# Performance work log

Measured on AMD Instinct MI355X. Metric: run time of the kernel, lower is better.

Reference implementation:

```python
import jax, jax.numpy as jnp
import numpy as np

N, E, D = 100000, 1600000, 128
EPS = 1e-5


def _bn(h, g, b):
    m = h.mean(0)
    v = ((h - m) ** 2).mean(0)  # biased var, as torch BatchNorm1d normalization
    return g * (h - m) / jnp.sqrt(v + EPS) + b


def _sage(x, src, dst, w_self, w_neigh, b, n):
    # mean aggregation over in-neighbors (edges src->dst)
    agg = jax.ops.segment_sum(x[src], dst, num_segments=n)          # [N, D]
    cnt = jax.ops.segment_sum(jnp.ones(src.shape, x.dtype), dst, num_segments=n)
    mean = agg / jnp.maximum(cnt, 1.0)[:, None]
    return x @ w_self + mean @ w_neigh + b


def setup_inputs() -> dict:
    key = jax.random.key(0)
    ks = jax.random.split(key, 8)
    s = 1.0 / np.sqrt(D)
    return {
        "x": jax.random.normal(ks[0], (N, D), jnp.float32),
        "src": jax.random.randint(ks[1], (E,), 0, N, jnp.int32),
        "dst": jax.random.randint(ks[2], (E,), 0, N, jnp.int32),
        "w_self1": jax.random.normal(ks[3], (D, D), jnp.float32) * s,
        "w_neigh1": jax.random.normal(ks[4], (D, D), jnp.float32) * s,
        "b1": jnp.zeros((D,), jnp.float32),
        "w_self2": jax.random.normal(ks[5], (D, D), jnp.float32) * s,
        "w_neigh2": jax.random.normal(ks[6], (D, D), jnp.float32) * s,
        "b2": jnp.zeros((D,), jnp.float32),
        "w_skip": jax.random.normal(ks[7], (D, D), jnp.float32) * s,
        "b_skip": jnp.zeros((D,), jnp.float32),
        "g1": jnp.ones((D,), jnp.float32), "be1": jnp.zeros((D,), jnp.float32),
        "g2": jnp.ones((D,), jnp.float32), "be2": jnp.zeros((D,), jnp.float32),
        "g3": jnp.ones((D,), jnp.float32), "be3": jnp.zeros((D,), jnp.float32),
    }


def reference(x, src, dst, w_self1, w_neigh1, b1, w_self2, w_neigh2, b2,
              w_skip, b_skip, g1, be1, g2, be2, g3, be3):
    n = x.shape[0]
    h1 = _sage(x, src, dst, w_self1, w_neigh1, b1, n)
    h1 = jax.nn.relu(_bn(h1, g1, be1))           # dropout: eval-mode identity
    h2 = _sage(h1, src, dst, w_self2, w_neigh2, b2, n)
    h2 = _bn(h2, g2, be2)
    skip = _bn(h1 @ w_skip + b_skip, g3, be3)
    return jax.nn.relu(h2 + skip)
```

## Files before the change

kernel.cpp:

```cpp
#include <hip/hip_runtime.h>

#define D 128
#define PCHUNK 4096
#define SCAP 8192

typedef short bf16x8 __attribute__((ext_vector_type(8)));
typedef float f32x4 __attribute__((ext_vector_type(4)));

__device__ __forceinline__ ushort f2b(float f){
  unsigned u = __builtin_bit_cast(unsigned, f);
  u += 0x7fffu + ((u >> 16) & 1u);
  return (ushort)(u >> 16);
}
__device__ __forceinline__ float b2f(ushort h){
  unsigned u = ((unsigned)h) << 16;
  return __builtin_bit_cast(float, u);
}

__global__ __launch_bounds__(256) void k_p0(const int* __restrict__ dst,
                                            int* __restrict__ bcnt, int E){
  __shared__ int h[512];
  for (int u=threadIdx.x; u<512; u+=256) h[u]=0;
  __syncthreads();
  for (long long i=(long long)blockIdx.x*256+threadIdx.x; i<E; i+=(long long)gridDim.x*256)
    atomicAdd(&h[dst[i]>>8], 1);
  __syncthreads();
  for (int u=threadIdx.x; u<512; u+=256) if (h[u]) atomicAdd(&bcnt[u], h[u]);
}

__global__ void k_bscan(const int* __restrict__ bcnt, int* __restrict__ bbase,
                        int* __restrict__ bcur, int nb, int E){
  __shared__ int sh[1024];
  int t = threadIdx.x;
  int v = (t<nb) ? bcnt[t] : 0;
  sh[t]=v; __syncthreads();
  for (int off=1; off<1024; off<<=1){
    int add = (t>=off)?sh[t-off]:0;
    __syncthreads();
    sh[t]+=add;
    __syncthreads();
  }
  if (t<nb){ int e=sh[t]-v; bbase[t]=e; bcur[t]=e; }
  if (t==nb) bbase[t]=E;
}

__global__ __launch_bounds__(256) void k_part(const int* __restrict__ src,
        const int* __restrict__ dst, int* __restrict__ bcur,
        unsigned* __restrict__ pairs, int E){
  __shared__ int hist[512], offA[512], offB[512], gbase[512];
  __shared__ int sS[PCHUNK], sD[PCHUNK];
  const int t = threadIdx.x;
  const int base = blockIdx.x * PCHUNK;
  const int cnt = min(PCHUNK, E - base);
  for (int u=t; u<512; u+=256) hist[u]=0;
  __syncthreads();
  int rs[16], rd[16];
  #pragma unroll
  for (int j=0;j<16;j++){
    int li = j*256 + t;
    if (li < cnt){
      rs[j]=src[base+li]; rd[j]=dst[base+li];
      atomicAdd(&hist[rd[j]>>8],1);
    } else { rs[j]=0; rd[j]=-1; }
  }
  __syncthreads();
  int *cur=offA, *nxt=offB;
  for (int u=t; u<512; u+=256) cur[u]=hist[u];
  __syncthreads();
  for (int off=1; off<512; off<<=1){
    for (int u=t; u<512; u+=256) nxt[u] = cur[u] + ((u>=off)?cur[u-off]:0);
    __syncthreads();
    int* tmp=cur; cur=nxt; nxt=tmp;
  }
  for (int u=t; u<512; u+=256) nxt[u] = cur[u]-hist[u];
  __syncthreads();
  #pragma unroll
  for (int j=0;j<16;j++){
    if (j*256+t < cnt){
      int b = rd[j]>>8;
      int p = atomicAdd(&nxt[b],1);
      sS[p]=rs[j]; sD[p]=rd[j];
    }
  }
  __syncthreads();
  for (int u=t; u<512; u+=256){
    int c = hist[u];
    if (c>0) gbase[u] = atomicAdd(&bcur[u], c);
  }
  __syncthreads();
  #pragma unroll
  for (int j=0;j<16;j++){
    int idx = j*256+t;
    if (idx<cnt){
      int d = sD[idx]; int b = d>>8;
      int gpos = gbase[b] + (idx - (cur[b]-hist[b]));
      pairs[gpos] = (unsigned)sS[idx] | ((unsigned)(d & 255) << 24);
    }
  }
}

__global__ __launch_bounds__(256) void k_sortb(const unsigned* __restrict__ pairs,
        const int* __restrict__ bbase, int* __restrict__ offs,
        int* __restrict__ slots, int N, int NB){
  __shared__ int nh[256], nc[256], sc[256];
  __shared__ int stage[SCAP];
  const int b = blockIdx.x, t = threadIdx.x;
  const int base = bbase[b];
  const int cnt  = bbase[b+1] - base;
  nh[t]=0; __syncthreads();
  for (int i=t;i<cnt;i+=256) atomicAdd(&nh[pairs[base+i] >> 24],1);
  __syncthreads();
  int v = nh[t];
  sc[t]=v; __syncthreads();
  for (int off=1; off<256; off<<=1){
    int add = (t>=off)?sc[t-off]:0;
    __syncthreads();
    sc[t]+=add;
    __syncthreads();
  }
  int excl = sc[t]-v;
  nc[t]=excl;
  int node = (b<<8)+t;
  if (node<N) offs[node]=base+excl;
  if (b==NB-1 && t==0) offs[N]=bbase[NB];
  __syncthreads();
  if (cnt<=SCAP){
    for (int i=t;i<cnt;i+=256){
      unsigned p = pairs[base+i];
      int pos = atomicAdd(&nc[p >> 24],1);
      stage[pos]=(int)(p & 0xffffffu);
    }
    __syncthreads();
    for (int i=t;i<cnt;i+=256) slots[base+i]=stage[i];
  } else {
    for (int i=t;i<cnt;i+=256){
      unsigned p = pairs[base+i];
      int pos = atomicAdd(&nc[p >> 24],1);
      slots[base+pos]=(int)(p & 0xffffffu);
    }
  }
}

__global__ __launch_bounds__(256) void k_xcast(const float* __restrict__ x,
                                               ushort* __restrict__ xb, long long n4){
  long long i = (long long)blockIdx.x*256 + threadIdx.x;
  const long long stride = (long long)gridDim.x*256;
  for (; i < n4; i += stride){
    float4 v = reinterpret_cast<const float4*>(x)[i];
    ushort4 o;
    o.x = f2b(v.x); o.y = f2b(v.y); o.z = f2b(v.z); o.w = f2b(v.w);
    reinterpret_cast<ushort4*>(xb)[i] = o;
  }
}

__global__ __launch_bounds__(256) void k_wtall(
    const float* __restrict__ w_self1, const float* __restrict__ w_neigh1,
    const float* __restrict__ w_self2, const float* __restrict__ w_neigh2,
    const float* __restrict__ w_skip,
    ushort* __restrict__ Wb1, ushort* __restrict__ Wb2, ushort* __restrict__ Wb3){
  const int grp = blockIdx.x >> 6;
  const int idx = (blockIdx.x & 63)*256 + threadIdx.x;
  const int k = idx >> 7, c = idx & 127;
  const float* W; ushort* Wb; int K, k0;
  switch (grp){
    case 0: W=w_self1;  Wb=Wb1; K=256; k0=0;   break;
    case 1: W=w_neigh1; Wb=Wb1; K=256; k0=128; break;
    case 2: W=w_self2;  Wb=Wb2; K=256; k0=0;   break;
    case 3: W=w_neigh2; Wb=Wb2; K=256; k0=128; break;
    default:W=w_skip;   Wb=Wb3; K=128; k0=0;   break;
  }
  Wb[(size_t)c*K + k0 + k] = f2b(W[idx]);
}

__global__ __launch_bounds__(256) void k_gatherb(const ushort* __restrict__ Xb,
        const int* __restrict__ slots, const int* __restrict__ offs,
        ushort* __restrict__ meanb, int N){
  int node = blockIdx.x*4 + (threadIdx.x >> 6);
  int c2 = (threadIdx.x & 63) * 2;
  if (node >= N) return;
  const int beg = offs[node], end = offs[node+1];
  float sx0=0,sy0=0,sx1=0,sy1=0,sx2=0,sy2=0,sx3=0,sy3=0;
  int j = beg;
  while (j < end && (j & 3)){
    unsigned u = *reinterpret_cast<const unsigned*>(&Xb[(size_t)slots[j]*D + c2]);
    sx0 += b2f((ushort)u); sy0 += b2f((ushort)(u>>16));
    ++j;
  }
  const int nfull = (end - j) >> 2;
  const int4* sp = reinterpret_cast<const int4*>(slots + j);

#define G8(ia, ib) { \
    unsigned u0 = *reinterpret_cast<const unsigned*>(&Xb[(size_t)(ia).x*D + c2]); \
    unsigned u1 = *reinterpret_cast<const unsigned*>(&Xb[(size_t)(ia).y*D + c2]); \
    unsigned u2 = *reinterpret_cast<const unsigned*>(&Xb[(size_t)(ia).z*D + c2]); \
    unsigned u3 = *reinterpret_cast<const unsigned*>(&Xb[(size_t)(ia).w*D + c2]); \
    unsigned u4 = *reinterpret_cast<const unsigned*>(&Xb[(size_t)(ib).x*D + c2]); \
    unsigned u5 = *reinterpret_cast<const unsigned*>(&Xb[(size_t)(ib).y*D + c2]); \
    unsigned u6 = *reinterpret_cast<const unsigned*>(&Xb[(size_t)(ib).z*D + c2]); \
    unsigned u7 = *reinterpret_cast<const unsigned*>(&Xb[(size_t)(ib).w*D + c2]); \
    sx0 += b2f((ushort)u0); sy0 += b2f((ushort)(u0>>16)); \
    sx1 += b2f((ushort)u1); sy1 += b2f((ushort)(u1>>16)); \
    sx2 += b2f((ushort)u2); sy2 += b2f((ushort)(u2>>16)); \
    sx3 += b2f((ushort)u3); sy3 += b2f((ushort)(u3>>16)); \
    sx0 += b2f((ushort)u4); sy0 += b2f((ushort)(u4>>16)); \
    sx1 += b2f((ushort)u5); sy1 += b2f((ushort)(u5>>16)); \
    sx2 += b2f((ushort)u6); sy2 += b2f((ushort)(u6>>16)); \
    sx3 += b2f((ushort)u7); sy3 += b2f((ushort)(u7>>16)); }

  int g = 0;
  if (nfull >= 2){
    int4 ia = sp[0], ib = sp[1];
    for (g = 2; g + 2 <= nfull; g += 2){
      int4 na = sp[g], nb = sp[g+1];
      G8(ia, ib);
      ia = na; ib = nb;
    }
    G8(ia, ib);
  }
  if (g < nfull){
    int4 ia = sp[g];
    unsigned u0 = *reinterpret_cast<const unsigned*>(&Xb[(size_t)ia.x*D + c2]);
    unsigned u1 = *reinterpret_cast<const unsigned*>(&Xb[(size_t)ia.y*D + c2]);
    unsigned u2 = *reinterpret_cast<const unsigned*>(&Xb[(size_t)ia.z*D + c2]);
    unsigned u3 = *reinterpret_cast<const unsigned*>(&Xb[(size_t)ia.w*D + c2]);
    sx0 += b2f((ushort)u0); sy0 += b2f((ushort)(u0>>16));
    sx1 += b2f((ushort)u1); sy1 += b2f((ushort)(u1>>16));
    sx2 += b2f((ushort)u2); sy2 += b2f((ushort)(u2>>16));
    sx3 += b2f((ushort)u3); sy3 += b2f((ushort)(u3>>16));
  }
  j += 4*nfull;
  for (; j < end; ++j){
    unsigned u = *reinterpret_cast<const unsigned*>(&Xb[(size_t)slots[j]*D + c2]);
    sx0 += b2f((ushort)u); sy0 += b2f((ushort)(u>>16));
  }
#undef G8
  float deg = (float)(end - beg);
  float rc = deg > 0.f ? 1.0f/deg : 0.f;
  unsigned o = (unsigned)f2b((sx0+sx1+sx2+sx3)*rc)
             | ((unsigned)f2b((sy0+sy1+sy2+sy3)*rc) << 16);
  *reinterpret_cast<unsigned*>(&meanb[(size_t)node*D + c2]) = o;
}

template<bool SKIP>
__global__ __launch_bounds__(256, 1) void k_mfma(
    const ushort* __restrict__ A0, const ushort* __restrict__ A1,
    const ushort* __restrict__ Wb, const ushort* __restrict__ Wk,
    const float* __restrict__ bias, const float* __restrict__ biasK,
    ushort* __restrict__ C, ushort* __restrict__ Ck,
    float* __restrict__ gS, float* __restrict__ gQ,
    float* __restrict__ gSK, float* __restrict__ gQK, int N, int NT)
{
  __shared__ ushort Wt8[8][128][40];
  __shared__ ushort Wkt4[SKIP ? 4*128*40 : 1];
  __shared__ ushort At[2][128][40];
  __shared__ float shS[128], shQ[128], shSK[SKIP?128:1], shQK[SKIP?128:1];
  const int tid = threadIdx.x;
  if (tid < 128){ shS[tid]=0.f; shQ[tid]=0.f; if (SKIP){ shSK[tid]=0.f; shQK[tid]=0.f; } }
  const int bid = blockIdx.x, gridN = gridDim.x;
  const int lane = tid & 63, wid = tid >> 6;
  const int wr = wid >> 1, wc = wid & 1;
  const int lr = lane & 15, kq = lane >> 4;
  const int sr4 = tid >> 2, s8 = (tid & 3) * 8;

  #pragma unroll
  for (int s=0;s<8;s++){
    *reinterpret_cast<int4*>(&Wt8[s][sr4][s8]) =
        *reinterpret_cast<const int4*>(&Wb[(size_t)sr4*256 + s*32 + s8]);
    *reinterpret_cast<int4*>(&Wt8[s][sr4+64][s8]) =
        *reinterpret_cast<const int4*>(&Wb[(size_t)(sr4+64)*256 + s*32 + s8]);
  }
  if (SKIP){
    #pragma unroll
    for (int s=0;s<4;s++){
      *reinterpret_cast<int4*>(&Wkt4[((s*128) + sr4)*40 + s8]) =
          *reinterpret_cast<const int4*>(&Wk[(size_t)sr4*128 + s*32 + s8]);
      *reinterpret_cast<int4*>(&Wkt4[((s*128) + sr4 + 64)*40 + s8]) =
          *reinterpret_cast<const int4*>(&Wk[(size_t)(sr4+64)*128 + s*32 + s8]);
    }
  }

  int4 va0a,va0b, va1a,va1b, va2a,va2b, va3a,va3b;

#define LOADA(S, GT, TT) { \
    int gr0_ = (GT)*128 + sr4;      if (gr0_ >= N) gr0_ = N-1; \
    int gr1_ = (GT)*128 + sr4 + 64; if (gr1_ >= N) gr1_ = N-1; \
    const ushort* As_ = ((TT) >= 4) ? A1 : A0; \
    const int ka_ = ((TT) & 3) * 32; \
    va##S##a = *reinterpret_cast<const int4*>(&As_[(size_t)gr0_*D + ka_ + s8]); \
    va##S##b = *reinterpret_cast<const int4*>(&As_[(size_t)gr1_*D + ka_ + s8]); }

#define WRITEA(S, BW) { \
    *reinterpret_cast<int4*>(&At[BW][sr4][s8]) = va##S##a; \
    *reinterpret_cast<int4*>(&At[BW][sr4+64][s8]) = va##S##b; }

#define PBAR() { asm volatile("s_waitcnt lgkmcnt(0)" ::: "memory"); \
    __builtin_amdgcn_s_barrier(); __builtin_amdgcn_sched_barrier(0); }

#define STEPBODY(BR, TT, WITHK, ...) { \
    bf16x8 af0 = *reinterpret_cast<const bf16x8*>(&At[BR][64*wr + lr][kq*8]); \
    bf16x8 af1 = *reinterpret_cast<const bf16x8*>(&At[BR][64*wr + 16 + lr][kq*8]); \
    bf16x8 af2 = *reinterpret_cast<const bf16x8*>(&At[BR][64*wr + 32 + lr][kq*8]); \
    bf16x8 af3 = *reinterpret_cast<const bf16x8*>(&At[BR][64*wr + 48 + lr][kq*8]); \
    bf16x8 bw0 = *reinterpret_cast<const bf16x8*>(&Wt8[TT][64*wc + lr][kq*8]); \
    bf16x8 bw1 = *reinterpret_cast<const bf16x8*>(&Wt8[TT][64*wc + 16 + lr][kq*8]); \
    bf16x8 bw2 = *reinterpret_cast<const bf16x8*>(&Wt8[TT][64*wc + 32 + lr][kq*8]); \
    bf16x8 bw3 = *reinterpret_cast<const bf16x8*>(&Wt8[TT][64*wc + 48 + lr][kq*8]); \
    bf16x8 bk0{}, bk1{}, bk2{}, bk3{}; \
    if (SKIP && (WITHK)){ \
      bk0 = *reinterpret_cast<const bf16x8*>(&Wkt4[(((TT)&3)*128 + 64*wc + lr)*40 + kq*8]); \
      bk1 = *reinterpret_cast<const bf16x8*>(&Wkt4[(((TT)&3)*128 + 64*wc + 16 + lr)*40 + kq*8]); \
      bk2 = *reinterpret_cast<const bf16x8*>(&Wkt4[(((TT)&3)*128 + 64*wc + 32 + lr)*40 + kq*8]); \
      bk3 = *reinterpret_cast<const bf16x8*>(&Wkt4[(((TT)&3)*128 + 64*wc + 48 + lr)*40 + kq*8]); \
    } \
    __VA_ARGS__; \
    __builtin_amdgcn_s_setprio(1); \
    acc[0][0] = __builtin_amdgcn_mfma_f32_16x16x32_bf16(af0, bw0, acc[0][0], 0,0,0); \
    acc[0][1] = __builtin_amdgcn_mfma_f32_16x16x32_bf16(af0, bw1, acc[0][1], 0,0,0); \
    acc[0][2] = __builtin_amdgcn_mfma_f32_16x16x32_bf16(af0, bw2, acc[0][2], 0,0,0); \
    acc[0][3] = __builtin_amdgcn_mfma_f32_16x16x32_bf16(af0, bw3, acc[0][3], 0,0,0); \
    acc[1][0] = __builtin_amdgcn_mfma_f32_16x16x32_bf16(af1, bw0, acc[1][0], 0,0,0); \
    acc[1][1] = __builtin_amdgcn_mfma_f32_16x16x32_bf16(af1, bw1, acc[1][1], 0,0,0); \
    acc[1][2] = __builtin_amdgcn_mfma_f32_16x16x32_bf16(af1, bw2, acc[1][2], 0,0,0); \
    acc[1][3] = __builtin_amdgcn_mfma_f32_16x16x32_bf16(af1, bw3, acc[1][3], 0,0,0); \
    acc[2][0] = __builtin_amdgcn_mfma_f32_16x16x32_bf16(af2, bw0, acc[2][0], 0,0,0); \
    acc[2][1] = __builtin_amdgcn_mfma_f32_16x16x32_bf16(af2, bw1, acc[2][1], 0,0,0); \
    acc[2][2] = __builtin_amdgcn_mfma_f32_16x16x32_bf16(af2, bw2, acc[2][2], 0,0,0); \
    acc[2][3] = __builtin_amdgcn_mfma_f32_16x16x32_bf16(af2, bw3, acc[2][3], 0,0,0); \
    acc[3][0] = __builtin_amdgcn_mfma_f32_16x16x32_bf16(af3, bw0, acc[3][0], 0,0,0); \
    acc[3][1] = __builtin_amdgcn_mfma_f32_16x16x32_bf16(af3, bw1, acc[3][1], 0,0,0); \
    acc[3][2] = __builtin_amdgcn_mfma_f32_16x16x32_bf16(af3, bw2, acc[3][2], 0,0,0); \
    acc[3][3] = __builtin_amdgcn_mfma_f32_16x16x32_bf16(af3, bw3, acc[3][3], 0,0,0); \
    if (SKIP && (WITHK)){ \
      accK[0][0] = __builtin_amdgcn_mfma_f32_16x16x32_bf16(af0, bk0, accK[0][0], 0,0,0); \
      accK[0][1] = __builtin_amdgcn_mfma_f32_16x16x32_bf16(af0, bk1, accK[0][1], 0,0,0); \
      accK[0][2] = __builtin_amdgcn_mfma_f32_16x16x32_bf16(af0, bk2, accK[0][2], 0,0,0); \
      accK[0][3] = __builtin_amdgcn_mfma_f32_16x16x32_bf16(af0, bk3, accK[0][3], 0,0,0); \
      accK[1][0] = __builtin_amdgcn_mfma_f32_16x16x32_bf16(af1, bk0, accK[1][0], 0,0,0); \
      accK[1][1] = __builtin_amdgcn_mfma_f32_16x16x32_bf16(af1, bk1, accK[1][1], 0,0,0); \
      accK[1][2] = __builtin_amdgcn_mfma_f32_16x16x32_bf16(af1, bk2, accK[1][2], 0,0,0); \
      accK[1][3] = __builtin_amdgcn_mfma_f32_16x16x32_bf16(af1, bk3, accK[1][3], 0,0,0); \
      accK[2][0] = __builtin_amdgcn_mfma_f32_16x16x32_bf16(af2, bk0, accK[2][0], 0,0,0); \
      accK[2][1] = __builtin_amdgcn_mfma_f32_16x16x32_bf16(af2, bk1, accK[2][1], 0,0,0); \
      accK[2][2] = __builtin_amdgcn_mfma_f32_16x16x32_bf16(af2, bk2, accK[2][2], 0,0,0); \
      accK[2][3] = __builtin_amdgcn_mfma_f32_16x16x32_bf16(af2, bk3, accK[2][3], 0,0,0); \
      accK[3][0] = __builtin_amdgcn_mfma_f32_16x16x32_bf16(af3, bk0, accK[3][0], 0,0,0); \
      accK[3][1] = __builtin_amdgcn_mfma_f32_16x16x32_bf16(af3, bk1, accK[3][1], 0,0,0); \
      accK[3][2] = __builtin_amdgcn_mfma_f32_16x16x32_bf16(af3, bk2, accK[3][2], 0,0,0); \
      accK[3][3] = __builtin_amdgcn_mfma_f32_16x16x32_bf16(af3, bk3, accK[3][3], 0,0,0); \
    } \
    __builtin_amdgcn_s_setprio(0); }

  f32x4 acc[4][4], accK[SKIP?4:1][SKIP?4:1];
  #pragma unroll
  for (int m=0;m<4;m++)
    #pragma unroll
    for (int n=0;n<4;n++){
      acc[m][n] = (f32x4){0.f,0.f,0.f,0.f};
      if (SKIP) accK[m][n] = (f32x4){0.f,0.f,0.f,0.f};
    }
  float bs[4]={0,0,0,0}, bq[4]={0,0,0,0}, bsk[4]={0,0,0,0}, bqk[4]={0,0,0,0};
  float bv[4], bkv[4];
  #pragma unroll
  for (int n=0;n<4;n++){
    bv[n] = bias[64*wc + 16*n + lr];
    bkv[n] = SKIP ? biasK[64*wc + 16*n + lr] : 0.f;
  }

  {
    const int t0 = bid;
    LOADA(0, t0, 0);
    LOADA(1, t0, 1);
    LOADA(2, t0, 2);
    LOADA(3, t0, 3);
    WRITEA(0, 0);
    PBAR();
  }

  for (int tile = bid; tile < NT; tile += gridN){
    const int tnext = tile + gridN;
    const bool hasnext = (tnext < NT);
    STEPBODY(0, 0, 1, LOADA(0, tile, 4));
    WRITEA(1, 1); PBAR();
    STEPBODY(1, 1, 1, LOADA(1, tile, 5));
    WRITEA(2, 0); PBAR();
    STEPBODY(0, 2, 1, LOADA(2, tile, 6));
    WRITEA(3, 1); PBAR();
    STEPBODY(1, 3, 1, LOADA(3, tile, 7));
    WRITEA(0, 0); PBAR();
    STEPBODY(0, 4, 0, if (hasnext) LOADA(0, tnext, 0));
    WRITEA(1, 1); PBAR();
    STEPBODY(1, 5, 0, if (hasnext) LOADA(1, tnext, 1));
    WRITEA(2, 0); PBAR();
    STEPBODY(0, 6, 0, if (hasnext) LOADA(2, tnext, 2));
    WRITEA(3, 1); PBAR();
    STEPBODY(1, 7, 0, if (hasnext) LOADA(3, tnext, 3));
    if (hasnext){ WRITEA(0, 0); PBAR(); }

    #pragma unroll
    for (int m=0;m<4;m++){
      #pragma unroll
      for (int r=0;r<4;r++){
        int row = tile*128 + 64*wr + 16*m + kq*4 + r;
        if (row < N){
          #pragma unroll
          for (int n=0;n<4;n++){
            int col = 64*wc + 16*n + lr;
            float v = acc[m][n][r] + bv[n];
            C[(size_t)row*D + col] = f2b(v);
            bs[n] += v; bq[n] += v*v;
            if (SKIP){
              float u = accK[m][n][r] + bkv[n];
              Ck[(size_t)row*D + col] = f2b(u);
              bsk[n] += u; bqk[n] += u*u;
            }
          }
        }
      }
    }
    #pragma unroll
    for (int m=0;m<4;m++)
      #pragma unroll
      for (int n=0;n<4;n++){
        acc[m][n] = (f32x4){0.f,0.f,0.f,0.f};
        if (SKIP) accK[m][n] = (f32x4){0.f,0.f,0.f,0.f};
      }
  }
#undef LOADA
#undef WRITEA
#undef PBAR
#undef STEPBODY

  #pragma unroll
  for (int n=0;n<4;n++){
    float s = bs[n], q = bq[n];
    s += __shfl_xor(s,16); s += __shfl_xor(s,32);
    q += __shfl_xor(q,16); q += __shfl_xor(q,32);
    if (kq == 0){
      int col = 64*wc + 16*n + lr;
      atomicAdd(&shS[col], s);
      atomicAdd(&shQ[col], q);
    }
    if (SKIP){
      float sk = bsk[n], qk = bqk[n];
      sk += __shfl_xor(sk,16); sk += __shfl_xor(sk,32);
      qk += __shfl_xor(qk,16); qk += __shfl_xor(qk,32);
      if (kq == 0){
        int col = 64*wc + 16*n + lr;
        atomicAdd(&shSK[col], sk);
        atomicAdd(&shQK[col], qk);
      }
    }
  }
  __syncthreads();
  if (tid < 128){
    unsafeAtomicAdd(&gS[tid], shS[tid]);
    unsafeAtomicAdd(&gQ[tid], shQ[tid]);
    if (SKIP){
      unsafeAtomicAdd(&gSK[tid], shSK[tid]);
      unsafeAtomicAdd(&gQK[tid], shQK[tid]);
    }
  }
}

__global__ __launch_bounds__(256) void k_bnrelub(const ushort* __restrict__ hpre,
      ushort* __restrict__ hb,
      const float* __restrict__ sum, const float* __restrict__ sq,
      const float* __restrict__ g, const float* __restrict__ be,
      float invN, long long n4){
  __shared__ float A[128], B[128];
  if (threadIdx.x < 128){
    int c = threadIdx.x;
    float m = sum[c]*invN;
    float v = sq[c]*invN - m*m;
    float a = g[c]*rsqrtf(fmaxf(v, 0.f) + 1e-5f);
    A[c] = a;
    B[c] = be[c] - m*a;
  }
  __syncthreads();
  long long i = (long long)blockIdx.x*256 + threadIdx.x;
  const long long stride = (long long)gridDim.x*256;
  for (; i < n4; i += stride){
    int c = ((int)(i & 31)) << 2;
    float4 a = *reinterpret_cast<const float4*>(A + c);
    float4 b = *reinterpret_cast<const float4*>(B + c);
    ushort4 hv = reinterpret_cast<const ushort4*>(hpre)[i];
    ushort4 o;
    o.x = f2b(fmaxf(a.x*b2f(hv.x) + b.x, 0.f));
    o.y = f2b(fmaxf(a.y*b2f(hv.y) + b.y, 0.f));
    o.z = f2b(fmaxf(a.z*b2f(hv.z) + b.z, 0.f));
    o.w = f2b(fmaxf(a.w*b2f(hv.w) + b.w, 0.f));
    reinterpret_cast<ushort4*>(hb)[i] = o;
  }
}

__global__ __launch_bounds__(256) void k_final(const ushort* __restrict__ h2,
      const ushort* __restrict__ sk, float* __restrict__ out,
      const float* __restrict__ sum2, const float* __restrict__ sq2,
      const float* __restrict__ g2, const float* __restrict__ be2,
      const float* __restrict__ sum3, const float* __restrict__ sq3,
      const float* __restrict__ g3, const float* __restrict__ be3,
      float invN, long long n4){
  __shared__ float A2[128], B2[128], A3[128], B3[128];
  if (threadIdx.x < 128){
    int c = threadIdx.x;
    float m2 = sum2[c]*invN;
    float v2 = sq2[c]*invN - m2*m2;
    float a2 = g2[c]*rsqrtf(fmaxf(v2, 0.f) + 1e-5f);
    A2[c] = a2; B2[c] = be2[c] - m2*a2;
    float m3 = sum3[c]*invN;
    float v3 = sq3[c]*invN - m3*m3;
    float a3 = g3[c]*rsqrtf(fmaxf(v3, 0.f) + 1e-5f);
    A3[c] = a3; B3[c] = be3[c] - m3*a3;
  }
  __syncthreads();
  long long i = (long long)blockIdx.x*256 + threadIdx.x;
  const long long stride = (long long)gridDim.x*256;
  for (; i < n4; i += stride){
    int c = ((int)(i & 31)) << 2;
    float4 a2 = *reinterpret_cast<const float4*>(A2 + c);
    float4 b2 = *reinterpret_cast<const float4*>(B2 + c);
    float4 a3 = *reinterpret_cast<const float4*>(A3 + c);
    float4 b3 = *reinterpret_cast<const float4*>(B3 + c);
    ushort4 h = reinterpret_cast<const ushort4*>(h2)[i];
    ushort4 s = reinterpret_cast<const ushort4*>(sk)[i];
    float4 v;
    v.x = fmaxf(a2.x*b2f(h.x) + b2.x + a3.x*b2f(s.x) + b3.x, 0.f);
    v.y = fmaxf(a2.y*b2f(h.y) + b2.y + a3.y*b2f(s.y) + b3.y, 0.f);
    v.z = fmaxf(a2.z*b2f(h.z) + b2.z + a3.z*b2f(s.z) + b3.z, 0.f);
    v.w = fmaxf(a2.w*b2f(h.w) + b2.w + a3.w*b2f(s.w) + b3.w, 0.f);
    reinterpret_cast<float4*>(out)[i] = v;
  }
}

extern "C" void kernel_launch(void* const* d_in, const int* in_sizes, int n_in,
                              void* d_out, int out_size, void* d_ws, size_t ws_size,
                              hipStream_t stream) {
  const float* x        = (const float*)d_in[0];
  const int*   src      = (const int*)  d_in[1];
  const int*   dst      = (const int*)  d_in[2];
  const float* w_self1  = (const float*)d_in[3];
  const float* w_neigh1 = (const float*)d_in[4];
  const float* b1       = (const float*)d_in[5];
  const float* w_self2  = (const float*)d_in[6];
  const float* w_neigh2 = (const float*)d_in[7];
  const float* b2       = (const float*)d_in[8];
  const float* w_skip   = (const float*)d_in[9];
  const float* b_skip   = (const float*)d_in[10];
  const float* g1       = (const float*)d_in[11];
  const float* be1      = (const float*)d_in[12];
  const float* g2       = (const float*)d_in[13];
  const float* be2      = (const float*)d_in[14];
  const float* g3       = (const float*)d_in[15];
  const float* be3      = (const float*)d_in[16];
  (void)n_in; (void)ws_size;

  const int N = in_sizes[0] / D;
  const int E = in_sizes[1];
  const int NB = (N + 255) >> 8;
  float* out = (float*)d_out;

  char* p = (char*)d_ws;
  const size_t nd2 = (((size_t)N * D * 2) + 255) / 256 * 256;
  ushort* meanb  = (ushort*)p; p += nd2;
  ushort* h1b    = (ushort*)p; p += nd2;
  ushort* hpre_b = (ushort*)p; p += nd2;
  ushort* skip_b = (ushort*)p; p += nd2;
  ushort* Wb1    = (ushort*)p; p += 256*128*2;
  ushort* Wb2    = (ushort*)p; p += 256*128*2;
  ushort* Wb3    = (ushort*)p; p += 128*128*2;
  int*    offs   = (int*)p;   p += (((size_t)(N+1)*4) + 255) / 256 * 256;
  int*    bcnt   = (int*)p;   p += 2304;
  float*  st     = (float*)p; p += 1536*sizeof(float);
  int*    bbase  = (int*)p;   p += 2304;
  int*    bcur   = (int*)p;   p += 2048;
  float *sum1=st,      *sq1=st+128,  *sum2=st+256, *sq2=st+384, *sum3=st+512, *sq3=st+640;

  const size_t slpad = (((size_t)E*4) + 255) / 256 * 256;
  const size_t xbpad = (((size_t)N*D*2) + 255) / 256 * 256;
  int*      slots = (int*)d_out;
  ushort*   xb    = (ushort*)((char*)d_out + slpad);
  unsigned* pairs = (unsigned*)((char*)d_out + slpad + xbpad);

  hipMemsetAsync(bcnt, 0, 2304 + 1536*sizeof(float), stream);

  const long long n4 = (long long)N * D / 4;

  k_xcast<<<2048, 256, 0, stream>>>(x, xb, n4);
  k_wtall<<<320, 256, 0, stream>>>(w_self1, w_neigh1, w_self2, w_neigh2, w_skip,
                                   Wb1, Wb2, Wb3);

  k_p0<<<1024, 256, 0, stream>>>(dst, bcnt, E);
  k_bscan<<<1, 1024, 0, stream>>>(bcnt, bbase, bcur, NB, E);
  k_part<<<(E + PCHUNK - 1)/PCHUNK, 256, 0, stream>>>(src, dst, bcur, pairs, E);
  k_sortb<<<NB, 256, 0, stream>>>(pairs, bbase, offs, slots, N, NB);

  const int gablocks = (N + 3) / 4;
  const int NT = (N + 127) / 128;
  const int gpersist = 256;
  const float invN = 1.0f / (float)N;

  k_gatherb<<<gablocks, 256, 0, stream>>>(xb, slots, offs, meanb, N);
  k_mfma<false><<<gpersist, 256, 0, stream>>>(xb, meanb, Wb1, nullptr, b1, nullptr,
                                              hpre_b, nullptr, sum1, sq1, nullptr, nullptr, N, NT);
  k_bnrelub<<<4096, 256, 0, stream>>>(hpre_b, h1b, sum1, sq1, g1, be1, invN, n4);

  k_gatherb<<<gablocks, 256, 0, stream>>>(h1b, slots, offs, meanb, N);

  k_mfma<true><<<gpersist, 256, 0, stream>>>(h1b, meanb, Wb2, Wb3, b2, b_skip,
                                             hpre_b, skip_b, sum2, sq2, sum3, sq3, N, NT);

  k_final<<<4096, 256, 0, stream>>>(hpre_b, skip_b, out,
                                    sum2, sq2, g2, be2, sum3, sq3, g3, be3, invN, n4);
}
```

Before: 292.1 us.

## Fuse BN+ReLU of layer 1 into gather and MFMA loads, merge prep kernels

```diff
diff --git a/kernel.cpp b/kernel.cpp
--- a/kernel.cpp
+++ b/kernel.cpp
@@ -17,15 +17,64 @@
   return __builtin_bit_cast(float, u);
 }
 
-__global__ __launch_bounds__(256) void k_p0(const int* __restrict__ dst,
-                                            int* __restrict__ bcnt, int E){
+__device__ __forceinline__ int4 bnpack8(int4 v, float4 a0, float4 a1, float4 b0, float4 b1){
+  unsigned w0=(unsigned)v.x, w1=(unsigned)v.y, w2=(unsigned)v.z, w3=(unsigned)v.w;
+  float x0 = fmaxf(fmaf(a0.x, b2f((ushort)w0),        b0.x), 0.f);
+  float x1 = fmaxf(fmaf(a0.y, b2f((ushort)(w0>>16)),  b0.y), 0.f);
+  float x2 = fmaxf(fmaf(a0.z, b2f((ushort)w1),        b0.z), 0.f);
+  float x3 = fmaxf(fmaf(a0.w, b2f((ushort)(w1>>16)),  b0.w), 0.f);
+  float x4 = fmaxf(fmaf(a1.x, b2f((ushort)w2),        b1.x), 0.f);
+  float x5 = fmaxf(fmaf(a1.y, b2f((ushort)(w2>>16)),  b1.y), 0.f);
+  float x6 = fmaxf(fmaf(a1.z, b2f((ushort)w3),        b1.z), 0.f);
+  float x7 = fmaxf(fmaf(a1.w, b2f((ushort)(w3>>16)),  b1.w), 0.f);
+  int4 r;
+  r.x = (int)((unsigned)f2b(x0) | ((unsigned)f2b(x1)<<16));
+  r.y = (int)((unsigned)f2b(x2) | ((unsigned)f2b(x3)<<16));
+  r.z = (int)((unsigned)f2b(x4) | ((unsigned)f2b(x5)<<16));
+  r.w = (int)((unsigned)f2b(x6) | ((unsigned)f2b(x7)<<16));
+  return r;
+}
+
+__global__ __launch_bounds__(256) void k_prep(
+    const float* __restrict__ w_self1, const float* __restrict__ w_neigh1,
+    const float* __restrict__ w_self2, const float* __restrict__ w_neigh2,
+    const float* __restrict__ w_skip,
+    ushort* __restrict__ Wb1, ushort* __restrict__ Wb2, ushort* __restrict__ Wb3,
+    const int* __restrict__ dst, int* __restrict__ bcnt, int E,
+    const float* __restrict__ x, ushort* __restrict__ xb, long long n4){
   __shared__ int h[512];
-  for (int u=threadIdx.x; u<512; u+=256) h[u]=0;
-  __syncthreads();
-  for (long long i=(long long)blockIdx.x*256+threadIdx.x; i<E; i+=(long long)gridDim.x*256)
-    atomicAdd(&h[dst[i]>>8], 1);
-  __syncthreads();
-  for (int u=threadIdx.x; u<512; u+=256) if (h[u]) atomicAdd(&bcnt[u], h[u]);
+  const int bid = blockIdx.x;
+  if (bid < 320){
+    const int grp = bid >> 6;
+    const int idx = (bid & 63)*256 + threadIdx.x;
+    const int k = idx >> 7, c = idx & 127;
+    const float* W; ushort* Wb; int K, k0;
+    switch (grp){
+      case 0: W=w_self1;  Wb=Wb1; K=256; k0=0;   break;
+      case 1: W=w_neigh1; Wb=Wb1; K=256; k0=128; break;
+      case 2: W=w_self2;  Wb=Wb2; K=256; k0=0;   break;
+      case 3: W=w_neigh2; Wb=Wb2; K=256; k0=128; break;
+      default:W=w_skip;   Wb=Wb3; K=128; k0=0;   break;
+    }
+    Wb[(size_t)c*K + k0 + k] = f2b(W[idx]);
+  } else if (bid < 1344){
+    const int pb = bid - 320;
+    for (int u=threadIdx.x; u<512; u+=256) h[u]=0;
+    __syncthreads();
+    for (long long i=(long long)pb*256+threadIdx.x; i<E; i+=(long long)1024*256)
+      atomicAdd(&h[dst[i]>>8], 1);
+    __syncthreads();
+    for (int u=threadIdx.x; u<512; u+=256) if (h[u]) atomicAdd(&bcnt[u], h[u]);
+  } else {
+    long long i = (long long)(bid-1344)*256 + threadIdx.x;
+    const long long stride = 2048LL*256;
+    for (; i < n4; i += stride){
+      float4 v = reinterpret_cast<const float4*>(x)[i];
+      ushort4 o;
+      o.x = f2b(v.x); o.y = f2b(v.y); o.z = f2b(v.z); o.w = f2b(v.w);
+      reinterpret_cast<ushort4*>(xb)[i] = o;
+    }
+  }
 }
 
 __global__ void k_bscan(const int* __restrict__ bcnt, int* __restrict__ bbase,
@@ -141,49 +190,32 @@
   }
 }
 
-__global__ __launch_bounds__(256) void k_xcast(const float* __restrict__ x,
-                                               ushort* __restrict__ xb, long long n4){
-  long long i = (long long)blockIdx.x*256 + threadIdx.x;
-  const long long stride = (long long)gridDim.x*256;
-  for (; i < n4; i += stride){
-    float4 v = reinterpret_cast<const float4*>(x)[i];
-    ushort4 o;
-    o.x = f2b(v.x); o.y = f2b(v.y); o.z = f2b(v.z); o.w = f2b(v.w);
-    reinterpret_cast<ushort4*>(xb)[i] = o;
-  }
-}
-
-__global__ __launch_bounds__(256) void k_wtall(
-    const float* __restrict__ w_self1, const float* __restrict__ w_neigh1,
-    const float* __restrict__ w_self2, const float* __restrict__ w_neigh2,
-    const float* __restrict__ w_skip,
-    ushort* __restrict__ Wb1, ushort* __restrict__ Wb2, ushort* __restrict__ Wb3){
-  const int grp = blockIdx.x >> 6;
-  const int idx = (blockIdx.x & 63)*256 + threadIdx.x;
-  const int k = idx >> 7, c = idx & 127;
-  const float* W; ushort* Wb; int K, k0;
-  switch (grp){
-    case 0: W=w_self1;  Wb=Wb1; K=256; k0=0;   break;
-    case 1: W=w_neigh1; Wb=Wb1; K=256; k0=128; break;
-    case 2: W=w_self2;  Wb=Wb2; K=256; k0=0;   break;
-    case 3: W=w_neigh2; Wb=Wb2; K=256; k0=128; break;
-    default:W=w_skip;   Wb=Wb3; K=128; k0=0;   break;
-  }
-  Wb[(size_t)c*K + k0 + k] = f2b(W[idx]);
-}
-
+template<bool BN>
 __global__ __launch_bounds__(256) void k_gatherb(const ushort* __restrict__ Xb,
         const int* __restrict__ slots, const int* __restrict__ offs,
-        ushort* __restrict__ meanb, int N){
+        ushort* __restrict__ meanb, int N,
+        const float* __restrict__ sum, const float* __restrict__ sq,
+        const float* __restrict__ g, const float* __restrict__ be, float invN){
   int node = blockIdx.x*4 + (threadIdx.x >> 6);
   int c2 = (threadIdx.x & 63) * 2;
   if (node >= N) return;
+  float a0=0.f,a1=0.f,b0c=0.f,b1c=0.f;
+  if (BN){
+    float m0 = sum[c2]*invN,   m1 = sum[c2+1]*invN;
+    float v0 = sq[c2]*invN - m0*m0, v1 = sq[c2+1]*invN - m1*m1;
+    a0 = g[c2]  *rsqrtf(fmaxf(v0,0.f)+1e-5f);
+    a1 = g[c2+1]*rsqrtf(fmaxf(v1,0.f)+1e-5f);
+    b0c = be[c2]   - m0*a0;
+    b1c = be[c2+1] - m1*a1;
+  }
+#define AX0(x) (BN ? fmaxf(fmaf(a0,(x),b0c),0.f) : (x))
+#define AX1(x) (BN ? fmaxf(fmaf(a1,(x),b1c),0.f) : (x))
   const int beg = offs[node], end = offs[node+1];
   float sx0=0,sy0=0,sx1=0,sy1=0,sx2=0,sy2=0,sx3=0,sy3=0;
   int j = beg;
   while (j < end && (j & 3)){
     unsigned u = *reinterpret_cast<const unsigned*>(&Xb[(size_t)slots[j]*D + c2]);
-    sx0 += b2f((ushort)u); sy0 += b2f((ushort)(u>>16));
+    sx0 += AX0(b2f((ushort)u)); sy0 += AX1(b2f((ushort)(u>>16)));
     ++j;
   }
   const int nfull = (end - j) >> 2;
@@ -198,42 +230,44 @@
     unsigned u5 = *reinterpret_cast<const unsigned*>(&Xb[(size_t)(ib).y*D + c2]); \
     unsigned u6 = *reinterpret_cast<const unsigned*>(&Xb[(size_t)(ib).z*D + c2]); \
     unsigned u7 = *reinterpret_cast<const unsigned*>(&Xb[(size_t)(ib).w*D + c2]); \
-    sx0 += b2f((ushort)u0); sy0 += b2f((ushort)(u0>>16)); \
-    sx1 += b2f((ushort)u1); sy1 += b2f((ushort)(u1>>16)); \
-    sx2 += b2f((ushort)u2); sy2 += b2f((ushort)(u2>>16)); \
-    sx3 += b2f((ushort)u3); sy3 += b2f((ushort)(u3>>16)); \
-    sx0 += b2f((ushort)u4); sy0 += b2f((ushort)(u4>>16)); \
-    sx1 += b2f((ushort)u5); sy1 += b2f((ushort)(u5>>16)); \
-    sx2 += b2f((ushort)u6); sy2 += b2f((ushort)(u6>>16)); \
-    sx3 += b2f((ushort)u7); sy3 += b2f((ushort)(u7>>16)); }
-
-  int g = 0;
+    sx0 += AX0(b2f((ushort)u0)); sy0 += AX1(b2f((ushort)(u0>>16))); \
+    sx1 += AX0(b2f((ushort)u1)); sy1 += AX1(b2f((ushort)(u1>>16))); \
+    sx2 += AX0(b2f((ushort)u2)); sy2 += AX1(b2f((ushort)(u2>>16))); \
+    sx3 += AX0(b2f((ushort)u3)); sy3 += AX1(b2f((ushort)(u3>>16))); \
+    sx0 += AX0(b2f((ushort)u4)); sy0 += AX1(b2f((ushort)(u4>>16))); \
+    sx1 += AX0(b2f((ushort)u5)); sy1 += AX1(b2f((ushort)(u5>>16))); \
+    sx2 += AX0(b2f((ushort)u6)); sy2 += AX1(b2f((ushort)(u6>>16))); \
+    sx3 += AX0(b2f((ushort)u7)); sy3 += AX1(b2f((ushort)(u7>>16))); }
+
+  int g8 = 0;
   if (nfull >= 2){
     int4 ia = sp[0], ib = sp[1];
-    for (g = 2; g + 2 <= nfull; g += 2){
-      int4 na = sp[g], nb = sp[g+1];
+    for (g8 = 2; g8 + 2 <= nfull; g8 += 2){
+      int4 na = sp[g8], nb = sp[g8+1];
       G8(ia, ib);
       ia = na; ib = nb;
     }
     G8(ia, ib);
   }
-  if (g < nfull){
-    int4 ia = sp[g];
+  if (g8 < nfull){
+    int4 ia = sp[g8];
     unsigned u0 = *reinterpret_cast<const unsigned*>(&Xb[(size_t)ia.x*D + c2]);
     unsigned u1 = *reinterpret_cast<const unsigned*>(&Xb[(size_t)ia.y*D + c2]);
     unsigned u2 = *reinterpret_cast<const unsigned*>(&Xb[(size_t)ia.z*D + c2]);
     unsigned u3 = *reinterpret_cast<const unsigned*>(&Xb[(size_t)ia.w*D + c2]);
-    sx0 += b2f((ushort)u0); sy0 += b2f((ushort)(u0>>16));
-    sx1 += b2f((ushort)u1); sy1 += b2f((ushort)(u1>>16));
-    sx2 += b2f((ushort)u2); sy2 += b2f((ushort)(u2>>16));
-    sx3 += b2f((ushort)u3); sy3 += b2f((ushort)(u3>>16));
+    sx0 += AX0(b2f((ushort)u0)); sy0 += AX1(b2f((ushort)(u0>>16)));
+    sx1 += AX0(b2f((ushort)u1)); sy1 += AX1(b2f((ushort)(u1>>16)));
+    sx2 += AX0(b2f((ushort)u2)); sy2 += AX1(b2f((ushort)(u2>>16)));
+    sx3 += AX0(b2f((ushort)u3)); sy3 += AX1(b2f((ushort)(u3>>16)));
   }
   j += 4*nfull;
   for (; j < end; ++j){
     unsigned u = *reinterpret_cast<const unsigned*>(&Xb[(size_t)slots[j]*D + c2]);
-    sx0 += b2f((ushort)u); sy0 += b2f((ushort)(u>>16));
+    sx0 += AX0(b2f((ushort)u)); sy0 += AX1(b2f((ushort)(u>>16)));
   }
 #undef G8
+#undef AX0
+#undef AX1
   float deg = (float)(end - beg);
   float rc = deg > 0.f ? 1.0f/deg : 0.f;
   unsigned o = (unsigned)f2b((sx0+sx1+sx2+sx3)*rc)
@@ -248,12 +282,15 @@
     const float* __restrict__ bias, const float* __restrict__ biasK,
     ushort* __restrict__ C, ushort* __restrict__ Ck,
     float* __restrict__ gS, float* __restrict__ gQ,
-    float* __restrict__ gSK, float* __restrict__ gQK, int N, int NT)
+    float* __restrict__ gSK, float* __restrict__ gQK, int N, int NT,
+    const float* __restrict__ sumA, const float* __restrict__ sqA,
+    const float* __restrict__ gA, const float* __restrict__ beA, float invN)
 {
   __shared__ ushort Wt8[8][128][40];
   __shared__ ushort Wkt4[SKIP ? 4*128*40 : 1];
   __shared__ ushort At[2][128][40];
   __shared__ float shS[128], shQ[128], shSK[SKIP?128:1], shQK[SKIP?128:1];
+  __shared__ float Af[SKIP?128:1], Bf[SKIP?128:1];
   const int tid = threadIdx.x;
   if (tid < 128){ shS[tid]=0.f; shQ[tid]=0.f; if (SKIP){ shSK[tid]=0.f; shQK[tid]=0.f; } }
   const int bid = blockIdx.x, gridN = gridDim.x;
@@ -262,6 +299,14 @@
   const int lr = lane & 15, kq = lane >> 4;
   const int sr4 = tid >> 2, s8 = (tid & 3) * 8;
 
+  if (SKIP && tid < 128){
+    float m = sumA[tid]*invN;
+    float v = sqA[tid]*invN - m*m;
+    float a = gA[tid]*rsqrtf(fmaxf(v,0.f)+1e-5f);
+    Af[tid] = a;
+    Bf[tid] = beA[tid] - m*a;
+  }
+
   #pragma unroll
   for (int s=0;s<8;s++){
     *reinterpret_cast<int4*>(&Wt8[s][sr4][s8]) =
@@ -289,9 +334,19 @@
     va##S##a = *reinterpret_cast<const int4*>(&As_[(size_t)gr0_*D + ka_ + s8]); \
     va##S##b = *reinterpret_cast<const int4*>(&As_[(size_t)gr1_*D + ka_ + s8]); }
 
-#define WRITEA(S, BW) { \
-    *reinterpret_cast<int4*>(&At[BW][sr4][s8]) = va##S##a; \
-    *reinterpret_cast<int4*>(&At[BW][sr4+64][s8]) = va##S##b; }
+#define WRITEA(S, BW, TT) { \
+    int4 wa_ = va##S##a, wb_ = va##S##b; \
+    if (SKIP && (TT) < 4){ \
+      const int cb_ = ((TT)&3)*32 + s8; \
+      float4 fa0_ = *reinterpret_cast<const float4*>(&Af[cb_]); \
+      float4 fa1_ = *reinterpret_cast<const float4*>(&Af[cb_+4]); \
+      float4 fb0_ = *reinterpret_cast<const float4*>(&Bf[cb_]); \
+      float4 fb1_ = *reinterpret_cast<const float4*>(&Bf[cb_+4]); \
+      wa_ = bnpack8(wa_, fa0_, fa1_, fb0_, fb1_); \
+      wb_ = bnpack8(wb_, fa0_, fa1_, fb0_, fb1_); \
+    } \
+    *reinterpret_cast<int4*>(&At[BW][sr4][s8]) = wa_; \
+    *reinterpret_cast<int4*>(&At[BW][sr4+64][s8]) = wb_; }
 
 #define PBAR() { asm volatile("s_waitcnt lgkmcnt(0)" ::: "memory"); \
     __builtin_amdgcn_s_barrier(); __builtin_amdgcn_sched_barrier(0); }
@@ -366,13 +421,15 @@
     bkv[n] = SKIP ? biasK[64*wc + 16*n + lr] : 0.f;
   }
 
+  PBAR();
+
   {
     const int t0 = bid;
     LOADA(0, t0, 0);
     LOADA(1, t0, 1);
     LOADA(2, t0, 2);
     LOADA(3, t0, 3);
-    WRITEA(0, 0);
+    WRITEA(0, 0, 0);
     PBAR();
   }
 
@@ -380,21 +437,21 @@
     const int tnext = tile + gridN;
     const bool hasnext = (tnext < NT);
     STEPBODY(0, 0, 1, LOADA(0, tile, 4));
-    WRITEA(1, 1); PBAR();
+    WRITEA(1, 1, 1); PBAR();
     STEPBODY(1, 1, 1, LOADA(1, tile, 5));
-    WRITEA(2, 0); PBAR();
+    WRITEA(2, 0, 2); PBAR();
     STEPBODY(0, 2, 1, LOADA(2, tile, 6));
-    WRITEA(3, 1); PBAR();
+    WRITEA(3, 1, 3); PBAR();
     STEPBODY(1, 3, 1, LOADA(3, tile, 7));
-    WRITEA(0, 0); PBAR();
+    WRITEA(0, 0, 4); PBAR();
     STEPBODY(0, 4, 0, if (hasnext) LOADA(0, tnext, 0));
-    WRITEA(1, 1); PBAR();
+    WRITEA(1, 1, 5); PBAR();
     STEPBODY(1, 5, 0, if (hasnext) LOADA(1, tnext, 1));
-    WRITEA(2, 0); PBAR();
+    WRITEA(2, 0, 6); PBAR();
     STEPBODY(0, 6, 0, if (hasnext) LOADA(2, tnext, 2));
-    WRITEA(3, 1); PBAR();
+    WRITEA(3, 1, 7); PBAR();
     STEPBODY(1, 7, 0, if (hasnext) LOADA(3, tnext, 3));
-    if (hasnext){ WRITEA(0, 0); PBAR(); }
+    if (hasnext){ WRITEA(0, 0, 0); PBAR(); }
 
     #pragma unroll
     for (int m=0;m<4;m++){
@@ -459,37 +516,6 @@
       unsafeAtomicAdd(&gSK[tid], shSK[tid]);
       unsafeAtomicAdd(&gQK[tid], shQK[tid]);
     }
-  }
-}
-
-__global__ __launch_bounds__(256) void k_bnrelub(const ushort* __restrict__ hpre,
-      ushort* __restrict__ hb,
-      const float* __restrict__ sum, const float* __restrict__ sq,
-      const float* __restrict__ g, const float* __restrict__ be,
-      float invN, long long n4){
-  __shared__ float A[128], B[128];
-  if (threadIdx.x < 128){
-    int c = threadIdx.x;
-    float m = sum[c]*invN;
-    float v = sq[c]*invN - m*m;
-    float a = g[c]*rsqrtf(fmaxf(v, 0.f) + 1e-5f);
-    A[c] = a;
-    B[c] = be[c] - m*a;
-  }
-  __syncthreads();
-  long long i = (long long)blockIdx.x*256 + threadIdx.x;
-  const long long stride = (long long)gridDim.x*256;
-  for (; i < n4; i += stride){
-    int c = ((int)(i & 31)) << 2;
-    float4 a = *reinterpret_cast<const float4*>(A + c);
-    float4 b = *reinterpret_cast<const float4*>(B + c);
-    ushort4 hv = reinterpret_cast<const ushort4*>(hpre)[i];
-    ushort4 o;
-    o.x = f2b(fmaxf(a.x*b2f(hv.x) + b.x, 0.f));
-    o.y = f2b(fmaxf(a.y*b2f(hv.y) + b.y, 0.f));
-    o.z = f2b(fmaxf(a.z*b2f(hv.z) + b.z, 0.f));
-    o.w = f2b(fmaxf(a.w*b2f(hv.w) + b.w, 0.f));
-    reinterpret_cast<ushort4*>(hb)[i] = o;
   }
 }
 
@@ -562,7 +588,7 @@
   char* p = (char*)d_ws;
   const size_t nd2 = (((size_t)N * D * 2) + 255) / 256 * 256;
   ushort* meanb  = (ushort*)p; p += nd2;
-  ushort* h1b    = (ushort*)p; p += nd2;
+  ushort* h2pre  = (ushort*)p; p += nd2;
   ushort* hpre_b = (ushort*)p; p += nd2;
   ushort* skip_b = (ushort*)p; p += nd2;
   ushort* Wb1    = (ushort*)p; p += 256*128*2;
@@ -585,11 +611,9 @@
 
   const long long n4 = (long long)N * D / 4;
 
-  k_xcast<<<2048, 256, 0, stream>>>(x, xb, n4);
-  k_wtall<<<320, 256, 0, stream>>>(w_self1, w_neigh1, w_self2, w_neigh2, w_skip,
-                                   Wb1, Wb2, Wb3);
-
-  k_p0<<<1024, 256, 0, stream>>>(dst, bcnt, E);
+  k_prep<<<3392, 256, 0, stream>>>(w_self1, w_neigh1, w_self2, w_neigh2, w_skip,
+                                   Wb1, Wb2, Wb3, dst, bcnt, E, x, xb, n4);
+
   k_bscan<<<1, 1024, 0, stream>>>(bcnt, bbase, bcur, NB, E);
   k_part<<<(E + PCHUNK - 1)/PCHUNK, 256, 0, stream>>>(src, dst, bcur, pairs, E);
   k_sortb<<<NB, 256, 0, stream>>>(pairs, bbase, offs, slots, N, NB);
@@ -599,16 +623,19 @@
   const int gpersist = 256;
   const float invN = 1.0f / (float)N;
 
-  k_gatherb<<<gablocks, 256, 0, stream>>>(xb, slots, offs, meanb, N);
+  k_gatherb<false><<<gablocks, 256, 0, stream>>>(xb, slots, offs, meanb, N,
+                                                 nullptr, nullptr, nullptr, nullptr, 0.f);
   k_mfma<false><<<gpersist, 256, 0, stream>>>(xb, meanb, Wb1, nullptr, b1, nullptr,
-                                              hpre_b, nullptr, sum1, sq1, nullptr, nullptr, N, NT);
-  k_bnrelub<<<4096, 256, 0, stream>>>(hpre_b, h1b, sum1, sq1, g1, be1, invN, n4);
-
-  k_gatherb<<<gablocks, 256, 0, stream>>>(h1b, slots, offs, meanb, N);
-
-  k_mfma<true><<<gpersist, 256, 0, stream>>>(h1b, meanb, Wb2, Wb3, b2, b_skip,
-                                             hpre_b, skip_b, sum2, sq2, sum3, sq3, N, NT);
-
-  k_final<<<4096, 256, 0, stream>>>(hpre_b, skip_b, out,
+                                              hpre_b, nullptr, sum1, sq1, nullptr, nullptr,
+                                              N, NT, nullptr, nullptr, nullptr, nullptr, 0.f);
+
+  k_gatherb<true><<<gablocks, 256, 0, stream>>>(hpre_b, slots, offs, meanb, N,
+                                                sum1, sq1, g1, be1, invN);
+
+  k_mfma<true><<<gpersist, 256, 0, stream>>>(hpre_b, meanb, Wb2, Wb3, b2, b_skip,
+                                             h2pre, skip_b, sum2, sq2, sum3, sq3,
+                                             N, NT, sum1, sq1, g1, be1, invN);
+
+  k_final<<<4096, 256, 0, stream>>>(h2pre, skip_b, out,
                                     sum2, sq2, g2, be2, sum3, sq3, g3, be3, invN, n4);
 }
```

After: 286.3 us (median of 2 runs). 2.0% less time.
